# Optimization experiments

Hardware: AMD Instinct MI355X
Metric: run time of the kernel (lower is better)

Reference implementation:

```python
import jax, jax.numpy as jnp
import numpy as np

N = 100000      # nodes
E = 1600000     # edges (avg degree 16)
D_IN, D_H, D_OUT = 128, 128, 40
BN_EPS = 1e-5


def _gcn_norm(edge_index):
    # add self-loops, compute symmetric normalization D^-1/2 (A+I) D^-1/2
    loops = jnp.arange(N, dtype=edge_index.dtype)
    src = jnp.concatenate([edge_index[0], loops])
    dst = jnp.concatenate([edge_index[1], loops])
    deg = jax.ops.segment_sum(jnp.ones(src.shape[0], jnp.float32), dst, num_segments=N)
    dinv = jnp.where(deg > 0, jax.lax.rsqrt(deg), 0.0)
    norm = dinv[src] * dinv[dst]  # [E+N]
    return src, dst, norm


def _gcn_conv(h, W, b, src, dst, norm):
    h = h @ W                          # [N, d_out]
    msg = h[src] * norm[:, None]       # [E+N, d_out] gather + scale
    out = jax.ops.segment_sum(msg, dst, num_segments=N)
    return out + b


def _bn(h, g, beta, mean, var):
    return g * (h - mean) * jax.lax.rsqrt(var + BN_EPS) + beta


def setup_inputs() -> dict:
    key = jax.random.key(0)
    ks = jax.random.split(key, 16)
    x = jax.random.normal(ks[0], (N, D_IN), jnp.float32)
    edge_index = jax.random.randint(ks[1], (2, E), 0, N, dtype=jnp.int32)
    s_in, s_h = 1.0 / np.sqrt(D_IN), 1.0 / np.sqrt(D_H)
    W0 = jax.random.normal(ks[2], (D_IN, D_H), jnp.float32) * s_in
    b0 = jnp.zeros((D_H,), jnp.float32)
    W1 = jax.random.normal(ks[3], (D_H, D_H), jnp.float32) * s_h
    b1 = jnp.zeros((D_H,), jnp.float32)
    W2 = jax.random.normal(ks[4], (D_H, D_OUT), jnp.float32) * s_h
    b2 = jnp.zeros((D_OUT,), jnp.float32)
    g0 = jnp.ones((D_H,), jnp.float32)
    be0 = jnp.zeros((D_H,), jnp.float32)
    m0 = jax.random.normal(ks[5], (D_H,), jnp.float32) * 0.1
    v0 = jax.random.uniform(ks[6], (D_H,), jnp.float32) + 0.5
    g1 = jnp.ones((D_H,), jnp.float32)
    be1 = jnp.zeros((D_H,), jnp.float32)
    m1 = jax.random.normal(ks[7], (D_H,), jnp.float32) * 0.1
    v1 = jax.random.uniform(ks[8], (D_H,), jnp.float32) + 0.5
    return {"x": x, "edge_index": edge_index,
            "W0": W0, "b0": b0, "W1": W1, "b1": b1, "W2": W2, "b2": b2,
            "g0": g0, "be0": be0, "m0": m0, "v0": v0,
            "g1": g1, "be1": be1, "m1": m1, "v1": v1}


def reference(x, edge_index, W0, b0, W1, b1, W2, b2,
              g0, be0, m0, v0, g1, be1, m1, v1):
    src, dst, norm = _gcn_norm(edge_index)
    h = _gcn_conv(x, W0, b0, src, dst, norm)
    h = jax.nn.relu(_bn(h, g0, be0, m0, v0))   # dropout = identity in eval
    h = _gcn_conv(h, W1, b1, src, dst, norm)
    h = jax.nn.relu(_bn(h, g1, be1, m1, v1))
    h = _gcn_conv(h, W2, b2, src, dst, norm)
    return jax.nn.log_softmax(h, axis=1)
```

## Files before the change

### kernel.cpp

```cpp
#include <hip/hip_runtime.h>
#include <math.h>


#define CSHIFT 9
#define CSZ 512
#define PCHUNK 4096

typedef unsigned short u16;
typedef unsigned int u32;
typedef unsigned char u8;
typedef float f32x4 __attribute__((ext_vector_type(4)));
typedef short s16x8 __attribute__((ext_vector_type(8)));

__device__ inline float bflo(u32 u) { return __uint_as_float(u << 16); }
__device__ inline float bfhi(u32 u) { return __uint_as_float(u & 0xffff0000u); }
__device__ inline u16 f2bf(float f) {
    u32 b = __float_as_uint(f);
    b += 0x7fff + ((b >> 16) & 1);
    return (u16)(b >> 16);
}
__device__ inline u32 pack2(float lo, float hi) {
    return (u32)f2bf(lo) | ((u32)f2bf(hi) << 16);
}


__global__ __launch_bounds__(256) void k_hist1(const int* __restrict__ dst,
                                               int* __restrict__ hist1,
                                               int E, int NB) {
    __shared__ int h[256];
    int t = threadIdx.x;
    h[t] = 0;
    __syncthreads();
    for (int i = blockIdx.x * 256 * 16 + t; i < min(E, (blockIdx.x + 1) * 256 * 16);
         i += 256)
        atomicAdd(&h[dst[i] >> CSHIFT], 1);
    __syncthreads();
    if (t < NB && h[t]) atomicAdd(&hist1[t], h[t]);
}

__global__ __launch_bounds__(256) void k_scan1(const int* __restrict__ hist1,
                                               int* __restrict__ base1,
                                               int* __restrict__ cur1,
                                               int NB, int E) {
    __shared__ int sc[256];
    int t = threadIdx.x;
    int v = (t < NB) ? hist1[t] : 0;
    sc[t] = v;
    __syncthreads();
    for (int d = 1; d < 256; d <<= 1) {
        int add = (t >= d) ? sc[t - d] : 0;
        __syncthreads();
        sc[t] += add;
        __syncthreads();
    }
    if (t < NB) {
        int excl = sc[t] - v;
        base1[t] = excl;
        cur1[t] = excl;
    }
    if (t == 0) base1[NB] = E;
}

__global__ __launch_bounds__(256) void k_part1(const int* __restrict__ src,
                                               const int* __restrict__ dst,
                                               int* __restrict__ cur1,
                                               u32* __restrict__ bkt,
                                               int E, int NB) {
    __shared__ u32 stage[PCHUNK];
    __shared__ u8 sbin[PCHUNK];
    __shared__ int cnt[256];
    __shared__ int lbase[256];
    __shared__ int lcur[256];
    __shared__ int gb[256];
    int t = threadIdx.x;
    int base = blockIdx.x * PCHUNK;
    int n = min(PCHUNK, E - base);
    cnt[t] = 0;
    __syncthreads();
    for (int i = t; i < n; i += 256) atomicAdd(&cnt[dst[base + i] >> CSHIFT], 1);
    __syncthreads();
    int v = cnt[t];
    lbase[t] = v;
    __syncthreads();
    for (int d = 1; d < 256; d <<= 1) {
        int add = (t >= d) ? lbase[t - d] : 0;
        __syncthreads();
        lbase[t] += add;
        __syncthreads();
    }
    {
        int excl = lbase[t] - v;
        __syncthreads();
        lbase[t] = excl;
        lcur[t] = excl;
        if (t < NB && v) gb[t] = atomicAdd(&cur1[t], v);
    }
    __syncthreads();
    for (int i = t; i < n; i += 256) {
        int d = dst[base + i];
        int s = src[base + i];
        int bin = d >> CSHIFT;
        int p = atomicAdd(&lcur[bin], 1);
        stage[p] = ((u32)s << CSHIFT) | (u32)(d & (CSZ - 1));
        sbin[p] = (u8)bin;
    }
    __syncthreads();
    for (int k = t; k < n; k += 256) {
        int bin = sbin[k];
        bkt[gb[bin] + (k - lbase[bin])] = stage[k];
    }
}

__global__ __launch_bounds__(1024) void k_csr(const u32* __restrict__ bkt,
                                              const int* __restrict__ base1,
                                              int* __restrict__ col,
                                              int* __restrict__ row,
                                              float* __restrict__ dinv,
                                              int N, int E) {
    __shared__ int deg[CSZ];
    __shared__ int cur[CSZ];
    int b = blockIdx.x;
    int t = threadIdx.x;
    int start = base1[b];
    int end = base1[b + 1];
    if (t < CSZ) deg[t] = 0;
    __syncthreads();
    for (int i = start + t; i < end; i += 1024)
        atomicAdd(&deg[bkt[i] & (CSZ - 1)], 1);
    __syncthreads();
    int v = (t < CSZ) ? deg[t] : 0;
    if (t < CSZ) cur[t] = v;
    __syncthreads();
    for (int d = 1; d < CSZ; d <<= 1) {
        int add = (t < CSZ && t >= d) ? cur[t - d] : 0;
        __syncthreads();
        if (t < CSZ) cur[t] += add;
        __syncthreads();
    }
    if (t < CSZ) {
        int excl = cur[t] - v;
        int node = (b << CSHIFT) + t;
        if (node < N) {
            row[node] = start + excl;
            dinv[node] = rsqrtf((float)(v + 1));
        }
        cur[t] = excl;
    }
    __syncthreads();
    for (int i = start + t; i < end; i += 1024) {
        u32 e = bkt[i];
        int p = start + atomicAdd(&cur[e & (CSZ - 1)], 1);
        col[p] = (int)(e >> CSHIFT);
    }
    if (b == 0 && t == 0) row[N] = E;
}


template <int NCT, int C>
__device__ inline void packW_elem(const float* __restrict__ W,
                                  u16* __restrict__ Wpk, int g) {
    int j = g & 7;
    int l = (g >> 3) & 63;
    int f = g >> 9;
    int ct = f % NCT, ks = f / NCT;
    int krow = ks * 32 + ((l >> 4) << 3) + j;
    int wcol = ct * 16 + (l & 15);
    Wpk[g] = (wcol < C) ? f2bf(W[krow * C + wcol]) : (u16)0;
}

__global__ __launch_bounds__(256) void k_packAll(const float* __restrict__ W0,
                                                 const float* __restrict__ W1,
                                                 const float* __restrict__ W2,
                                                 u16* __restrict__ Wpk0,
                                                 u16* __restrict__ Wpk1,
                                                 u16* __restrict__ Wpk2) {
    int b = blockIdx.x;
    int t = threadIdx.x;
    if (b < 64) {
        packW_elem<8, 128>(W0, Wpk0, b * 256 + t);
    } else if (b < 128) {
        packW_elem<8, 128>(W1, Wpk1, (b - 64) * 256 + t);
    } else {
        int g = (b - 128) * 256 + t;
        if (g < 12 * 512) packW_elem<3, 40>(W2, Wpk2, g);
    }
}


template <bool AFP32, int NCT>
__global__ __launch_bounds__(256) void k_gemmN(const void* __restrict__ Av,
                                               const u16* __restrict__ Wpk,
                                               u16* __restrict__ C,
                                               const float* __restrict__ dinv,
                                               int M, int ostride) {
    int tid = threadIdx.x;
    int wv = blockIdx.x * 4 + (tid >> 6);
    int rowbase = wv * 16;
    if (rowbase >= M) return;
    int l = tid & 63;
    int r = l & 15, hi = l >> 4;

    f32x4 acc[NCT];
#pragma unroll
    for (int ct = 0; ct < NCT; ++ct) acc[ct] = (f32x4)(0.f);

    const uint4* wp = (const uint4*)Wpk;
#pragma unroll
    for (int ks = 0; ks < 4; ++ks) {
        s16x8 afrag;
        int abase = (min(rowbase + r, M - 1)) * 128 + ks * 32 + hi * 8;
        if (AFP32) {
            const float* A = (const float*)Av;
            float4 a0 = *(const float4*)&A[abase];
            float4 a1 = *(const float4*)&A[abase + 4];
            uint4 u = make_uint4(pack2(a0.x, a0.y), pack2(a0.z, a0.w),
                                 pack2(a1.x, a1.y), pack2(a1.z, a1.w));
            afrag = *(s16x8*)&u;
        } else {
            const u16* A = (const u16*)Av;
            uint4 u = *(const uint4*)&A[abase];
            afrag = *(s16x8*)&u;
        }
#pragma unroll
        for (int ct = 0; ct < NCT; ++ct) {
            uint4 b = wp[(ks * NCT + ct) * 64 + l];
            s16x8 bfrag = *(s16x8*)&b;
            acc[ct] = __builtin_amdgcn_mfma_f32_16x16x32_bf16(afrag, bfrag, acc[ct], 0, 0, 0);
        }
    }
#pragma unroll
    for (int ct = 0; ct < NCT; ++ct) {
#pragma unroll
        for (int reg = 0; reg < 4; ++reg) {
            int orow = rowbase + 4 * hi + reg;
            int oc = ct * 16 + r;
            if (orow < M && oc < ostride)
                C[(size_t)orow * ostride + oc] = f2bf(dinv[orow] * acc[ct][reg]);
        }
    }
}


__global__ __launch_bounds__(256) void k_agg128(const u16* __restrict__ X,
                                                u16* __restrict__ Y,
                                                const int* __restrict__ row,
                                                const int* __restrict__ col,
                                                const float* __restrict__ dinv,
                                                const float* __restrict__ bias,
                                                const float* __restrict__ g,
                                                const float* __restrict__ be,
                                                const float* __restrict__ mean,
                                                const float* __restrict__ var,
                                                int n) {
    int tid = threadIdx.x;
    int wid = tid >> 6, lane = tid & 63;
    int half = lane >> 5, l5 = lane & 31;
    int node = (blockIdx.x * 4 + wid) * 2 + half;
    bool valid = node < n;
    int nc = valid ? node : (n - 1);
    const uint2* xp = (const uint2*)X;
    int s = row[nc], e = row[nc + 1];
    uint2 v = xp[(size_t)nc * 32 + l5];
    float a0 = bflo(v.x), a1 = bfhi(v.x), a2 = bflo(v.y), a3 = bfhi(v.y);
    float b0 = 0, b1 = 0, b2 = 0, b3 = 0;
    float c0 = 0, c1 = 0, c2 = 0, c3 = 0;
    float d0 = 0, d1 = 0, d2 = 0, d3 = 0;
    int j = s;
    for (; j + 8 <= e; j += 8) {
        int e0 = col[j], e1 = col[j+1], e2 = col[j+2], e3 = col[j+3];
        int e4 = col[j+4], e5 = col[j+5], e6 = col[j+6], e7 = col[j+7];
        uint2 x0 = xp[(size_t)e0 * 32 + l5];
        uint2 x1 = xp[(size_t)e1 * 32 + l5];
        uint2 x2 = xp[(size_t)e2 * 32 + l5];
        uint2 x3 = xp[(size_t)e3 * 32 + l5];
        uint2 x4 = xp[(size_t)e4 * 32 + l5];
        uint2 x5 = xp[(size_t)e5 * 32 + l5];
        uint2 x6 = xp[(size_t)e6 * 32 + l5];
        uint2 x7 = xp[(size_t)e7 * 32 + l5];
        a0 += bflo(x0.x); a1 += bfhi(x0.x); a2 += bflo(x0.y); a3 += bfhi(x0.y);
        b0 += bflo(x1.x); b1 += bfhi(x1.x); b2 += bflo(x1.y); b3 += bfhi(x1.y);
        c0 += bflo(x2.x); c1 += bfhi(x2.x); c2 += bflo(x2.y); c3 += bfhi(x2.y);
        d0 += bflo(x3.x); d1 += bfhi(x3.x); d2 += bflo(x3.y); d3 += bfhi(x3.y);
        a0 += bflo(x4.x); a1 += bfhi(x4.x); a2 += bflo(x4.y); a3 += bfhi(x4.y);
        b0 += bflo(x5.x); b1 += bfhi(x5.x); b2 += bflo(x5.y); b3 += bfhi(x5.y);
        c0 += bflo(x6.x); c1 += bfhi(x6.x); c2 += bflo(x6.y); c3 += bfhi(x6.y);
        d0 += bflo(x7.x); d1 += bfhi(x7.x); d2 += bflo(x7.y); d3 += bfhi(x7.y);
    }
    for (; j + 2 <= e; j += 2) {
        int e0 = col[j], e1 = col[j+1];
        uint2 x0 = xp[(size_t)e0 * 32 + l5];
        uint2 x1 = xp[(size_t)e1 * 32 + l5];
        a0 += bflo(x0.x); a1 += bfhi(x0.x); a2 += bflo(x0.y); a3 += bfhi(x0.y);
        b0 += bflo(x1.x); b1 += bfhi(x1.x); b2 += bflo(x1.y); b3 += bfhi(x1.y);
    }
    if (j < e) {
        uint2 x0 = xp[(size_t)col[j] * 32 + l5];
        c0 += bflo(x0.x); c1 += bfhi(x0.x); c2 += bflo(x0.y); c3 += bfhi(x0.y);
    }
    float dv = dinv[nc];
    float s0 = dv * ((a0 + b0) + (c0 + d0));
    float s1 = dv * ((a1 + b1) + (c1 + d1));
    float s2 = dv * ((a2 + b2) + (c2 + d2));
    float s3 = dv * ((a3 + b3) + (c3 + d3));
    float4 g4 = ((const float4*)g)[l5];
    float4 be4 = ((const float4*)be)[l5];
    float4 m4 = ((const float4*)mean)[l5];
    float4 v4 = ((const float4*)var)[l5];
    float4 bi4 = ((const float4*)bias)[l5];
    float sc0 = g4.x * rsqrtf(v4.x + 1e-5f);
    float sc1 = g4.y * rsqrtf(v4.y + 1e-5f);
    float sc2 = g4.z * rsqrtf(v4.z + 1e-5f);
    float sc3 = g4.w * rsqrtf(v4.w + 1e-5f);
    float y0 = fmaxf(fmaf(sc0, s0, fmaf(sc0, bi4.x - m4.x, be4.x)), 0.f);
    float y1 = fmaxf(fmaf(sc1, s1, fmaf(sc1, bi4.y - m4.y, be4.y)), 0.f);
    float y2 = fmaxf(fmaf(sc2, s2, fmaf(sc2, bi4.z - m4.z, be4.z)), 0.f);
    float y3 = fmaxf(fmaf(sc3, s3, fmaf(sc3, bi4.w - m4.w, be4.w)), 0.f);
    if (valid) {
        uint2 o;
        o.x = pack2(y0, y1);
        o.y = pack2(y2, y3);
        ((uint2*)Y)[(size_t)node * 32 + l5] = o;
    }
}

__global__ __launch_bounds__(256) void k_agg40(const u16* __restrict__ X,
                                               float* __restrict__ out,
                                               const int* __restrict__ row,
                                               const int* __restrict__ col,
                                               const float* __restrict__ dinv,
                                               const float* __restrict__ b2,
                                               int n) {
    int tid = threadIdx.x;
    int wid = tid >> 6, lane = tid & 63;
    int grp = lane >> 4, li = lane & 15;
    int node = (blockIdx.x * 4 + wid) * 4 + grp;
    bool valid = node < n;
    int nc = valid ? node : (n - 1);
    bool active = li < 10;
    int liw = min(li, 9);
    const uint2* xp = (const uint2*)X;
    int s = row[nc], e = row[nc + 1];

    uint2 v = xp[(size_t)nc * 10 + liw];
    float a0 = bflo(v.x), a1 = bfhi(v.x), a2 = bflo(v.y), a3 = bfhi(v.y);
    float b0 = 0, b1 = 0, b2_ = 0, b3 = 0;
    float c0 = 0, c1 = 0, c2 = 0, c3 = 0;
    float d0 = 0, d1 = 0, d2 = 0, d3 = 0;
    int j = s;
    for (; j + 8 <= e; j += 8) {
        int e0 = col[j], e1 = col[j+1], e2 = col[j+2], e3 = col[j+3];
        int e4 = col[j+4], e5 = col[j+5], e6 = col[j+6], e7 = col[j+7];
        uint2 x0 = xp[(size_t)e0 * 10 + liw];
        uint2 x1 = xp[(size_t)e1 * 10 + liw];
        uint2 x2 = xp[(size_t)e2 * 10 + liw];
        uint2 x3 = xp[(size_t)e3 * 10 + liw];
        uint2 x4 = xp[(size_t)e4 * 10 + liw];
        uint2 x5 = xp[(size_t)e5 * 10 + liw];
        uint2 x6 = xp[(size_t)e6 * 10 + liw];
        uint2 x7 = xp[(size_t)e7 * 10 + liw];
        a0 += bflo(x0.x); a1 += bfhi(x0.x); a2 += bflo(x0.y); a3 += bfhi(x0.y);
        b0 += bflo(x1.x); b1 += bfhi(x1.x); b2_ += bflo(x1.y); b3 += bfhi(x1.y);
        c0 += bflo(x2.x); c1 += bfhi(x2.x); c2 += bflo(x2.y); c3 += bfhi(x2.y);
        d0 += bflo(x3.x); d1 += bfhi(x3.x); d2 += bflo(x3.y); d3 += bfhi(x3.y);
        a0 += bflo(x4.x); a1 += bfhi(x4.x); a2 += bflo(x4.y); a3 += bfhi(x4.y);
        b0 += bflo(x5.x); b1 += bfhi(x5.x); b2_ += bflo(x5.y); b3 += bfhi(x5.y);
        c0 += bflo(x6.x); c1 += bfhi(x6.x); c2 += bflo(x6.y); c3 += bfhi(x6.y);
        d0 += bflo(x7.x); d1 += bfhi(x7.x); d2 += bflo(x7.y); d3 += bfhi(x7.y);
    }
    for (; j + 2 <= e; j += 2) {
        int e0 = col[j], e1 = col[j+1];
        uint2 x0 = xp[(size_t)e0 * 10 + liw];
        uint2 x1 = xp[(size_t)e1 * 10 + liw];
        a0 += bflo(x0.x); a1 += bfhi(x0.x); a2 += bflo(x0.y); a3 += bfhi(x0.y);
        b0 += bflo(x1.x); b1 += bfhi(x1.x); b2_ += bflo(x1.y); b3 += bfhi(x1.y);
    }
    if (j < e) {
        uint2 x0 = xp[(size_t)col[j] * 10 + liw];
        c0 += bflo(x0.x); c1 += bfhi(x0.x); c2 += bflo(x0.y); c3 += bfhi(x0.y);
    }
    float dv = dinv[nc];
    float y0 = -INFINITY, y1 = -INFINITY, y2 = -INFINITY, y3 = -INFINITY;
    if (active) {
        float4 bb = ((const float4*)b2)[liw];
        y0 = fmaf(dv, (a0 + b0) + (c0 + d0), bb.x);
        y1 = fmaf(dv, (a1 + b1) + (c1 + d1), bb.y);
        y2 = fmaf(dv, (a2 + b2_) + (c2 + d2), bb.z);
        y3 = fmaf(dv, (a3 + b3) + (c3 + d3), bb.w);
    }
    float m = fmaxf(fmaxf(y0, y1), fmaxf(y2, y3));
#pragma unroll
    for (int d = 8; d; d >>= 1) m = fmaxf(m, __shfl_xor(m, d));
    float ex = 0.f;
    if (active)
        ex = (__expf(y0 - m) + __expf(y1 - m)) + (__expf(y2 - m) + __expf(y3 - m));
#pragma unroll
    for (int d = 8; d; d >>= 1) ex += __shfl_xor(ex, d);
    if (valid && active) {
        float lse = m + __logf(ex);
        ((float4*)out)[(size_t)node * 10 + li] =
            make_float4(y0 - lse, y1 - lse, y2 - lse, y3 - lse);
    }
}


extern "C" void kernel_launch(void* const* d_in, const int* in_sizes, int n_in,
                              void* d_out, int out_size, void* d_ws, size_t ws_size,
                              hipStream_t stream) {
    const float* x   = (const float*)d_in[0];
    const int*   ei  = (const int*)d_in[1];
    const float* W0  = (const float*)d_in[2];
    const float* b0  = (const float*)d_in[3];
    const float* W1  = (const float*)d_in[4];
    const float* b1  = (const float*)d_in[5];
    const float* W2  = (const float*)d_in[6];
    const float* b2  = (const float*)d_in[7];
    const float* g0  = (const float*)d_in[8];
    const float* be0 = (const float*)d_in[9];
    const float* m0  = (const float*)d_in[10];
    const float* v0  = (const float*)d_in[11];
    const float* g1  = (const float*)d_in[12];
    const float* be1 = (const float*)d_in[13];
    const float* m1  = (const float*)d_in[14];
    const float* v1  = (const float*)d_in[15];
    float* out = (float*)d_out;

    int N = in_sizes[0] / 128;
    int E = in_sizes[1] / 2;
    const int* src = ei;
    const int* dst = ei + E;

    int NB = (N + CSZ - 1) / CSZ;

    char* ws = (char*)d_ws;
    size_t off = 0;
    auto alloc = [&](size_t bytes) -> char* {
        char* p = ws + off;
        off += (bytes + 255) & ~(size_t)255;
        return p;
    };
    u16*   XsA   = (u16*)alloc((size_t)N * 128 * 2);
    u16*   XsB   = (u16*)alloc((size_t)N * 128 * 2);
    u16*   bufC  = (u16*)alloc((size_t)N * 40 * 2);
    int*   col   = (int*)alloc((size_t)E * 4 + 64);
    int*   row   = (int*)alloc((size_t)(N + 1) * 4);
    float* dinv  = (float*)alloc((size_t)N * 4);
    int*   hist1 = (int*)alloc((size_t)(NB + 1) * 4);
    int*   base1 = (int*)alloc((size_t)(NB + 1) * 4);
    int*   cur1  = (int*)alloc((size_t)(NB + 1) * 4);
    u16*   Wpk0  = (u16*)alloc(128 * 128 * 2);
    u16*   Wpk1  = (u16*)alloc(128 * 128 * 2);
    u16*   Wpk2  = (u16*)alloc(128 * 48 * 2);
    u32*   bkt   = (u32*)XsA;

    hipError_t _e = hipMemsetAsync(hist1, 0, (size_t)(NB + 1) * 4, stream);
    (void)_e;
    k_hist1<<<(E + 4095) / 4096, 256, 0, stream>>>(dst, hist1, E, NB);
    k_scan1<<<1, 256, 0, stream>>>(hist1, base1, cur1, NB, E);
    k_part1<<<(E + PCHUNK - 1) / PCHUNK, 256, 0, stream>>>(src, dst, cur1, bkt, E, NB);
    k_csr<<<NB, 1024, 0, stream>>>(bkt, base1, col, row, dinv, N, E);
    k_packAll<<<152, 256, 0, stream>>>(W0, W1, W2, Wpk0, Wpk1, Wpk2);

    int gemmGrid = ((N + 15) / 16 + 3) / 4;
    k_gemmN<true, 8><<<gemmGrid, 256, 0, stream>>>(x, Wpk0, XsA, dinv, N, 128);
    k_agg128<<<(N + 7) / 8, 256, 0, stream>>>(XsA, XsB, row, col, dinv, b0, g0, be0, m0, v0, N);
    k_gemmN<false, 8><<<gemmGrid, 256, 0, stream>>>(XsB, Wpk1, XsA, dinv, N, 128);
    k_agg128<<<(N + 7) / 8, 256, 0, stream>>>(XsA, XsB, row, col, dinv, b1, g1, be1, m1, v1, N);
    k_gemmN<false, 3><<<gemmGrid, 256, 0, stream>>>(XsB, Wpk2, bufC, dinv, N, 40);
    k_agg40<<<(N + 15) / 16, 256, 0, stream>>>(bufC, out, row, col, dinv, b2, N);
}
```

Baseline: 277.9 us.

## Fuse histogram, scan and weight packing into one launch with last-block scan

```diff
diff --git a/kernel.cpp b/kernel.cpp
--- a/kernel.cpp
+++ b/kernel.cpp
@@ -24,27 +24,73 @@
 }
 
 
-__global__ __launch_bounds__(256) void k_hist1(const int* __restrict__ dst,
-                                               int* __restrict__ hist1,
-                                               int E, int NB) {
+template <int NCT, int C>
+__device__ inline void packW_elem(const float* __restrict__ W,
+                                  u16* __restrict__ Wpk, int g) {
+    int j = g & 7;
+    int l = (g >> 3) & 63;
+    int f = g >> 9;
+    int ct = f % NCT, ks = f / NCT;
+    int krow = ks * 32 + ((l >> 4) << 3) + j;
+    int wcol = ct * 16 + (l & 15);
+    Wpk[g] = (wcol < C) ? f2bf(W[krow * C + wcol]) : (u16)0;
+}
+
+
+__global__ __launch_bounds__(256) void k_build1(const int* __restrict__ dst,
+                                                int* __restrict__ hist1,
+                                                int* __restrict__ ctr,
+                                                int* __restrict__ base1,
+                                                int* __restrict__ cur1,
+                                                const float* __restrict__ W0,
+                                                const float* __restrict__ W1,
+                                                const float* __restrict__ W2,
+                                                u16* __restrict__ Wpk0,
+                                                u16* __restrict__ Wpk1,
+                                                u16* __restrict__ Wpk2,
+                                                int E, int NB, int HG) {
+    int b = blockIdx.x;
+    int t = threadIdx.x;
+    if (b >= HG) {
+        int pb = b - HG;
+        if (pb < 64) {
+            packW_elem<8, 128>(W0, Wpk0, pb * 256 + t);
+        } else if (pb < 128) {
+            packW_elem<8, 128>(W1, Wpk1, (pb - 64) * 256 + t);
+        } else {
+            int g = (pb - 128) * 256 + t;
+            if (g < 12 * 512) packW_elem<3, 40>(W2, Wpk2, g);
+        }
+        return;
+    }
     __shared__ int h[256];
-    int t = threadIdx.x;
+    __shared__ bool amLast;
     h[t] = 0;
     __syncthreads();
-    for (int i = blockIdx.x * 256 * 16 + t; i < min(E, (blockIdx.x + 1) * 256 * 16);
-         i += 256)
-        atomicAdd(&h[dst[i] >> CSHIFT], 1);
+    int base = b * PCHUNK;
+    int n = min(PCHUNK, E - base);
+    int n4 = n >> 2;
+    const int4* d4 = (const int4*)(dst + base);
+    for (int i = t; i < n4; i += 256) {
+        int4 v = d4[i];
+        atomicAdd(&h[v.x >> CSHIFT], 1);
+        atomicAdd(&h[v.y >> CSHIFT], 1);
+        atomicAdd(&h[v.z >> CSHIFT], 1);
+        atomicAdd(&h[v.w >> CSHIFT], 1);
+    }
+    for (int i = (n4 << 2) + t; i < n; i += 256)
+        atomicAdd(&h[dst[base + i] >> CSHIFT], 1);
     __syncthreads();
     if (t < NB && h[t]) atomicAdd(&hist1[t], h[t]);
-}
-
-__global__ __launch_bounds__(256) void k_scan1(const int* __restrict__ hist1,
-                                               int* __restrict__ base1,
-                                               int* __restrict__ cur1,
-                                               int NB, int E) {
+    __threadfence();
+    __syncthreads();
+    if (t == 0) amLast = (atomicAdd(ctr, 1) == HG - 1);
+    __syncthreads();
+    if (!amLast) return;
     __shared__ int sc[256];
-    int t = threadIdx.x;
-    int v = (t < NB) ? hist1[t] : 0;
+    int v = 0;
+    if (t < NB)
+        v = __hip_atomic_load(&hist1[t], __ATOMIC_RELAXED, __HIP_MEMORY_SCOPE_AGENT);
     sc[t] = v;
     __syncthreads();
     for (int d = 1; d < 256; d <<= 1) {
@@ -61,7 +107,8 @@
     if (t == 0) base1[NB] = E;
 }
 
-__global__ __launch_bounds__(256) void k_part1(const int* __restrict__ src,
+
+__global__ __launch_bounds__(512) void k_part1(const int* __restrict__ src,
                                                const int* __restrict__ dst,
                                                int* __restrict__ cur1,
                                                u32* __restrict__ bkt,
@@ -75,28 +122,37 @@
     int t = threadIdx.x;
     int base = blockIdx.x * PCHUNK;
     int n = min(PCHUNK, E - base);
-    cnt[t] = 0;
-    __syncthreads();
-    for (int i = t; i < n; i += 256) atomicAdd(&cnt[dst[base + i] >> CSHIFT], 1);
-    __syncthreads();
-    int v = cnt[t];
-    lbase[t] = v;
+    if (t < 256) cnt[t] = 0;
+    __syncthreads();
+    int n4 = n >> 2;
+    const int4* d4 = (const int4*)(dst + base);
+    for (int i = t; i < n4; i += 512) {
+        int4 v = d4[i];
+        atomicAdd(&cnt[v.x >> CSHIFT], 1);
+        atomicAdd(&cnt[v.y >> CSHIFT], 1);
+        atomicAdd(&cnt[v.z >> CSHIFT], 1);
+        atomicAdd(&cnt[v.w >> CSHIFT], 1);
+    }
+    for (int i = (n4 << 2) + t; i < n; i += 512)
+        atomicAdd(&cnt[dst[base + i] >> CSHIFT], 1);
+    __syncthreads();
+    int v = (t < 256) ? cnt[t] : 0;
+    if (t < 256) lbase[t] = v;
     __syncthreads();
     for (int d = 1; d < 256; d <<= 1) {
-        int add = (t >= d) ? lbase[t - d] : 0;
-        __syncthreads();
-        lbase[t] += add;
-        __syncthreads();
-    }
-    {
+        int add = (t < 256 && t >= d) ? lbase[t - d] : 0;
+        __syncthreads();
+        if (t < 256) lbase[t] += add;
+        __syncthreads();
+    }
+    if (t < 256) {
         int excl = lbase[t] - v;
-        __syncthreads();
         lbase[t] = excl;
         lcur[t] = excl;
         if (t < NB && v) gb[t] = atomicAdd(&cur1[t], v);
     }
     __syncthreads();
-    for (int i = t; i < n; i += 256) {
+    for (int i = t; i < n; i += 512) {
         int d = dst[base + i];
         int s = src[base + i];
         int bin = d >> CSHIFT;
@@ -105,7 +161,7 @@
         sbin[p] = (u8)bin;
     }
     __syncthreads();
-    for (int k = t; k < n; k += 256) {
+    for (int k = t; k < n; k += 512) {
         int bin = sbin[k];
         bkt[gb[bin] + (k - lbase[bin])] = stage[k];
     }
@@ -153,37 +209,6 @@
         col[p] = (int)(e >> CSHIFT);
     }
     if (b == 0 && t == 0) row[N] = E;
-}
-
-
-template <int NCT, int C>
-__device__ inline void packW_elem(const float* __restrict__ W,
-                                  u16* __restrict__ Wpk, int g) {
-    int j = g & 7;
-    int l = (g >> 3) & 63;
-    int f = g >> 9;
-    int ct = f % NCT, ks = f / NCT;
-    int krow = ks * 32 + ((l >> 4) << 3) + j;
-    int wcol = ct * 16 + (l & 15);
-    Wpk[g] = (wcol < C) ? f2bf(W[krow * C + wcol]) : (u16)0;
-}
-
-__global__ __launch_bounds__(256) void k_packAll(const float* __restrict__ W0,
-                                                 const float* __restrict__ W1,
-                                                 const float* __restrict__ W2,
-                                                 u16* __restrict__ Wpk0,
-                                                 u16* __restrict__ Wpk1,
-                                                 u16* __restrict__ Wpk2) {
-    int b = blockIdx.x;
-    int t = threadIdx.x;
-    if (b < 64) {
-        packW_elem<8, 128>(W0, Wpk0, b * 256 + t);
-    } else if (b < 128) {
-        packW_elem<8, 128>(W1, Wpk1, (b - 64) * 256 + t);
-    } else {
-        int g = (b - 128) * 256 + t;
-        if (g < 12 * 512) packW_elem<3, 40>(W2, Wpk2, g);
-    }
 }
 
 
@@ -430,6 +455,7 @@
     const int* dst = ei + E;
 
     int NB = (N + CSZ - 1) / CSZ;
+    int HG = (E + PCHUNK - 1) / PCHUNK;
 
     char* ws = (char*)d_ws;
     size_t off = 0;
@@ -444,21 +470,21 @@
     int*   col   = (int*)alloc((size_t)E * 4 + 64);
     int*   row   = (int*)alloc((size_t)(N + 1) * 4);
     float* dinv  = (float*)alloc((size_t)N * 4);
-    int*   hist1 = (int*)alloc((size_t)(NB + 1) * 4);
+    int*   hist1 = (int*)alloc((size_t)(NB + 2) * 4);
     int*   base1 = (int*)alloc((size_t)(NB + 1) * 4);
     int*   cur1  = (int*)alloc((size_t)(NB + 1) * 4);
     u16*   Wpk0  = (u16*)alloc(128 * 128 * 2);
     u16*   Wpk1  = (u16*)alloc(128 * 128 * 2);
     u16*   Wpk2  = (u16*)alloc(128 * 48 * 2);
     u32*   bkt   = (u32*)XsA;
-
-    hipError_t _e = hipMemsetAsync(hist1, 0, (size_t)(NB + 1) * 4, stream);
+    int*   ctr   = hist1 + NB + 1;
+
+    hipError_t _e = hipMemsetAsync(hist1, 0, (size_t)(NB + 2) * 4, stream);
     (void)_e;
-    k_hist1<<<(E + 4095) / 4096, 256, 0, stream>>>(dst, hist1, E, NB);
-    k_scan1<<<1, 256, 0, stream>>>(hist1, base1, cur1, NB, E);
-    k_part1<<<(E + PCHUNK - 1) / PCHUNK, 256, 0, stream>>>(src, dst, cur1, bkt, E, NB);
+    k_build1<<<HG + 152, 256, 0, stream>>>(dst, hist1, ctr, base1, cur1,
+                                           W0, W1, W2, Wpk0, Wpk1, Wpk2, E, NB, HG);
+    k_part1<<<HG, 512, 0, stream>>>(src, dst, cur1, bkt, E, NB);
     k_csr<<<NB, 1024, 0, stream>>>(bkt, base1, col, row, dinv, N, E);
-    k_packAll<<<152, 256, 0, stream>>>(W0, W1, W2, Wpk0, Wpk1, Wpk2);
 
     int gemmGrid = ((N + 15) / 16 + 3) / 4;
     k_gemmN<true, 8><<<gemmGrid, 256, 0, stream>>>(x, Wpk0, XsA, dinv, N, 128);
```

Result: slower. 285.8 us (+2.8%).
